# Optimization experiments

Hardware: AMD Instinct MI355X
Metric: run time of the kernel (lower is better)

Reference implementation:

```python
import jax, jax.numpy as jnp
import numpy as np

NUM_HEADS = 16
HEAD_SIZE = 64
CTXT_LEN = 2048
N_EMBED = 1024
BATCH = 2


def setup_inputs() -> dict:
    key = jax.random.key(0)
    ks = jax.random.split(key, 5)
    s = 0.02  # realistic init scale for weights
    return {
        "x": jax.random.normal(ks[0], (BATCH, CTXT_LEN, N_EMBED), dtype=jnp.float32),
        "Wk": jax.random.normal(ks[1], (N_EMBED, NUM_HEADS * HEAD_SIZE), dtype=jnp.float32) * s,
        "bk": jnp.zeros((NUM_HEADS * HEAD_SIZE,), dtype=jnp.float32),
        "Wq": jax.random.normal(ks[2], (N_EMBED, NUM_HEADS * HEAD_SIZE), dtype=jnp.float32) * s,
        "bq": jnp.zeros((NUM_HEADS * HEAD_SIZE,), dtype=jnp.float32),
        "Wv": jax.random.normal(ks[3], (N_EMBED, NUM_HEADS * HEAD_SIZE), dtype=jnp.float32) * s,
        "bv": jnp.zeros((NUM_HEADS * HEAD_SIZE,), dtype=jnp.float32),
        "Wo": jax.random.normal(ks[4], (NUM_HEADS * HEAD_SIZE, N_EMBED), dtype=jnp.float32) * s,
        "bo": jnp.zeros((N_EMBED,), dtype=jnp.float32),
    }


def reference(x, Wk, bk, Wq, bq, Wv, bv, Wo, bo):
    B, T, E = x.shape
    H, D = NUM_HEADS, HEAD_SIZE
    # QKV projections -> [B, T, H, D]
    k = (x @ Wk + bk).reshape(B, T, H, D)
    q = (x @ Wq + bq).reshape(B, T, H, D)
    v = (x @ Wv + bv).reshape(B, T, H, D)
    # NOTE: source scales by 1/sqrt(n_embed), not 1/sqrt(head_size)
    scale = 1.0 / (E ** 0.5)
    wei = jnp.einsum('bthd,bshd->bhts', q, k) * scale  # [B, H, T, T]
    causal = jnp.tril(jnp.ones((T, T), dtype=bool))
    wei = jnp.where(causal, wei, -jnp.inf)
    wei = jax.nn.softmax(wei, axis=-1)
    # dropout p=0.0 -> identity
    out = jnp.einsum('bhts,bshd->bthd', wei, v).reshape(B, T, H * D)
    return out @ Wo + bo
```

## Files before the change

### kernel.cpp

```cpp
#include <hip/hip_runtime.h>

#define NH 16
#define HS 64
#define T_CTX 2048
#define NE 1024
#define NB 2
#define BT (NB*T_CTX)
#define HD (NH*HS)

typedef unsigned short u16;
typedef __bf16 bf16_t;
typedef bf16_t bf16x8 __attribute__((ext_vector_type(8)));
typedef float f32x4 __attribute__((ext_vector_type(4)));
typedef u16 u16x8 __attribute__((ext_vector_type(8)));
typedef u16 u16x4 __attribute__((ext_vector_type(4)));

#define GLDS(gp, lp) __builtin_amdgcn_global_load_lds( \
    (const __attribute__((address_space(1))) void*)(gp), \
    (__attribute__((address_space(3))) void*)(lp), 16, 0, 0)

__device__ __forceinline__ u16 f2bf(float f) {
  union { float f; unsigned u; } x; x.f = f;
  return (u16)((x.u + 0x7fffu + ((x.u >> 16) & 1u)) >> 16);
}
__device__ __forceinline__ float bf2f(u16 u) {
  union { unsigned u; float f; } x; x.u = ((unsigned)u) << 16;
  return x.f;
}
__device__ __forceinline__ unsigned pack_bf2(float hi, float lo) {
  union { float f; unsigned u; } H, L; H.f = hi; L.f = lo;
  return __builtin_amdgcn_perm(H.u + 0x8000u, L.u + 0x8000u, 0x07060302);
}

__global__ __launch_bounds__(256) void k_prep_x(const float* __restrict__ x,
                                                u16* __restrict__ xb) {
  int i = blockIdx.x * blockDim.x + threadIdx.x;
  float4 v = ((const float4*)x)[i];
  ushort4 o;
  o.x = f2bf(v.x); o.y = f2bf(v.y); o.z = f2bf(v.z); o.w = f2bf(v.w);
  ((ushort4*)xb)[i] = o;
}

__global__ __launch_bounds__(256) void k_prep_w(
    const float* __restrict__ W0, const float* __restrict__ W1,
    const float* __restrict__ W2, const float* __restrict__ W3,
    u16* __restrict__ T0, u16* __restrict__ T1,
    u16* __restrict__ T2, u16* __restrict__ T3) {
  const float* W; u16* T;
  switch (blockIdx.z) {
    case 0: W = W0; T = T0; break;
    case 1: W = W1; T = T1; break;
    case 2: W = W2; T = T2; break;
    default: W = W3; T = T3; break;
  }
  __shared__ u16 tile[64 * 72];
  int k0 = blockIdx.x * 64, n0 = blockIdx.y * 64;
  int tid = threadIdx.x;
#pragma unroll
  for (int it = 0; it < 4; ++it) {
    int ci = tid + it * 256;
    int k = ci >> 4, c = ci & 15;
    float4 v = *(const float4*)&W[(size_t)(k0 + k) * NE + n0 + c * 4];
    int n = c * 4;
    tile[(n + 0) * 72 + k] = f2bf(v.x);
    tile[(n + 1) * 72 + k] = f2bf(v.y);
    tile[(n + 2) * 72 + k] = f2bf(v.z);
    tile[(n + 3) * 72 + k] = f2bf(v.w);
  }
  __syncthreads();
#pragma unroll
  for (int it = 0; it < 2; ++it) {
    int co = tid + it * 256;
    int n = co >> 3, c = co & 7;
    u16x8 v = *(const u16x8*)&tile[n * 72 + c * 8];
    *(u16x8*)&T[(size_t)(n0 + n) * NE + k0 + c * 8] = v;
  }
}

__device__ __forceinline__ void gemm_core(
    const u16* __restrict__ A, const u16* __restrict__ Bt,
    int m0, int n0, u16* As, u16* Bs, f32x4 (&acc)[4][4]) {
  const int tid = threadIdx.x, lane = tid & 63, w = tid >> 6;
  const int wm = (w >> 1) * 64, wn = (w & 1) * 64;
  const int q = lane >> 4, l16 = lane & 15;
#pragma unroll
  for (int i = 0; i < 4; ++i)
#pragma unroll
    for (int j = 0; j < 4; ++j)
#pragma unroll
      for (int r = 0; r < 4; ++r) acc[i][j][r] = 0.f;

  for (int k0 = 0; k0 < NE; k0 += 32) {
#pragma unroll
    for (int s2 = 0; s2 < 2; ++s2) {
      int ci = w * 64 + lane + s2 * 256;
      int row = ci >> 2, cc = ci & 3;
      GLDS(A  + (size_t)(m0 + row) * NE + k0 + cc * 8, As + (size_t)(w * 64 + s2 * 256) * 8);
      GLDS(Bt + (size_t)(n0 + row) * NE + k0 + cc * 8, Bs + (size_t)(w * 64 + s2 * 256) * 8);
    }
    __syncthreads();
    bf16x8 av[4], bv4[4];
#pragma unroll
    for (int i = 0; i < 4; ++i) av[i]  = *(const bf16x8*)&As[(wm + i * 16 + l16) * 32 + q * 8];
#pragma unroll
    for (int j = 0; j < 4; ++j) bv4[j] = *(const bf16x8*)&Bs[(wn + j * 16 + l16) * 32 + q * 8];
#pragma unroll
    for (int i = 0; i < 4; ++i)
#pragma unroll
      for (int j = 0; j < 4; ++j)
        acc[i][j] = __builtin_amdgcn_mfma_f32_16x16x32_bf16(av[i], bv4[j], acc[i][j], 0, 0, 0);
    __syncthreads();
  }
}

__global__ __launch_bounds__(256) void k_gemm_qkv(
    const u16* __restrict__ xb, const u16* __restrict__ Wt,
    const float* __restrict__ bq, const float* __restrict__ bk,
    const float* __restrict__ bv, u16* __restrict__ Qw,
    u16* __restrict__ Kw, u16* __restrict__ Vtw) {
  __shared__ u16 As[128 * 32], Bs[128 * 32];
  __shared__ u16 Es[128 * 132];
  const int z = blockIdx.z;
  const u16* W = Wt + (size_t)z * NE * HD;
  const float* bias = (z == 0) ? bq : (z == 1 ? bk : bv);
  const float scale = (z == 0) ? 0.03125f * 1.4426950408889634f : 1.0f;
  const int m0 = blockIdx.y * 128, n0 = blockIdx.x * 128;
  f32x4 acc[4][4];
  gemm_core(xb, W, m0, n0, As, Bs, acc);
  const int tid = threadIdx.x;
  const int lane = tid & 63, w = tid >> 6;
  const int wm = (w >> 1) * 64, wn = (w & 1) * 64, q = lane >> 4, l16 = lane & 15;
  const int bb = m0 >> 11;
  if (z == 2) {
#pragma unroll
    for (int j = 0; j < 4; ++j) {
      int n = wn + j * 16 + l16;
      float bn = bias[n0 + n];
#pragma unroll
      for (int i = 0; i < 4; ++i) {
        int m = wm + i * 16 + q * 4;
        u16x4 pk;
#pragma unroll
        for (int r = 0; r < 4; ++r) pk[r] = f2bf(acc[i][j][r] + bn);
        *(u16x4*)&Es[n * 132 + m] = pk;
      }
    }
    __syncthreads();
#pragma unroll
    for (int it = 0; it < 8; ++it) {
      int idx = it * 256 + tid;
      int dl = idx >> 4, c = idx & 15;
      u16x8 v = *(const u16x8*)&Es[dl * 132 + c * 8];
      int ng = n0 + dl, h = ng >> 6, d = ng & 63;
      int tt = (m0 & (T_CTX - 1)) + c * 8;
      *(u16x8*)&Vtw[((size_t)((bb * NH + h) * HS + d)) * T_CTX + tt] = v;
    }
  } else {
    u16* dst = (z == 0) ? Qw : Kw;
#pragma unroll
    for (int j = 0; j < 4; ++j) {
      int n = wn + j * 16 + l16;
      float bn = bias[n0 + n];
#pragma unroll
      for (int i = 0; i < 4; ++i)
#pragma unroll
        for (int r = 0; r < 4; ++r) {
          int m = wm + i * 16 + q * 4 + r;
          Es[m * 132 + n] = f2bf((acc[i][j][r] + bn) * scale);
        }
    }
    __syncthreads();
#pragma unroll
    for (int it = 0; it < 8; ++it) {
      int idx = it * 256 + tid;
      int tl = idx >> 4, c = idx & 15;
      u16x8 v = *(const u16x8*)&Es[tl * 132 + c * 8];
      int ng = n0 + c * 8, h = ng >> 6, d = ng & 63;
      int tt = (m0 & (T_CTX - 1)) + tl;
      *(u16x8*)&dst[(((size_t)(bb * NH + h)) * T_CTX + tt) * HS + d] = v;
    }
  }
}

__device__ __forceinline__ void stage_kv(const u16* __restrict__ Kp,
                                         const u16* __restrict__ Vp,
                                         int k0, u16* KsB, u16* VsB, int tid) {
#pragma unroll
  for (int it = 0; it < 2; ++it) {
    int ci = tid + it * 256;
    int row = ci >> 3, cc = ci & 7;
    int prow = (row & 32) | ((row & 12) << 1) | ((row & 16) >> 2) | (row & 3);
    int sw = (cc ^ (row & 7)) * 8;
    GLDS(Kp + (size_t)(k0 + prow) * HS + sw, KsB + ci * 8);
    GLDS(Vp + (size_t)row * T_CTX + k0 + sw, VsB + ci * 8);
  }
}

__global__ __launch_bounds__(256) void k_attn(
    const u16* __restrict__ Qw, const u16* __restrict__ Kw,
    const u16* __restrict__ Vtw, u16* __restrict__ op0,
    u16* __restrict__ op1, u16* __restrict__ op2,
    float* __restrict__ lsum) {
  __shared__ u16 Ks[3 * 64 * 64];
  __shared__ u16 Vs[3 * 64 * 64];

  const int bh = blockIdx.y;
  const int x = blockIdx.x;
  const int qt = 15 - x / 3;
  const int part = x - (15 - qt) * 3;
  const int ntiles = 2 * (qt + 1);
  const int npt = (ntiles + 2) / 3;
  const int klo = part * npt;
  const int khi = min(klo + npt, ntiles);
  const int qbase = qt * 128;

  const u16* Qp = Qw + (size_t)bh * T_CTX * HS;
  const u16* Kp = Kw + (size_t)bh * T_CTX * HS;
  const u16* Vp = Vtw + (size_t)bh * HS * T_CTX;

  const int tid = threadIdx.x, lane = tid & 63, w = tid >> 6;
  const int q = lane >> 4, c = lane & 15;
  const int rbase = w * 32;

  bf16x8 aq[2][2];
#pragma unroll
  for (int i = 0; i < 2; ++i)
#pragma unroll
    for (int s = 0; s < 2; ++s)
      aq[i][s] = *(const bf16x8*)&Qp[(size_t)(qbase + rbase + i * 16 + c) * HS + s * 32 + q * 8];

  f32x4 o[2][4];
  float lrow[2] = {0.f, 0.f};
#pragma unroll
  for (int i = 0; i < 2; ++i)
#pragma unroll
    for (int j = 0; j < 4; ++j)
#pragma unroll
      for (int r = 0; r < 4; ++r) o[i][j][r] = 0.f;

  if (klo < khi)     stage_kv(Kp, Vp, klo * 64,       Ks,        Vs,        tid);
  if (klo + 1 < khi) stage_kv(Kp, Vp, (klo + 1) * 64, Ks + 4096, Vs + 4096, tid);

  for (int kt = klo; kt < khi; ++kt) {
    const int k0 = kt * 64;
    const int idx = kt - klo;
    u16* KsB = Ks + (idx % 3) * 4096;
    u16* VsB = Vs + (idx % 3) * 4096;
    if (kt + 1 < khi) {
      asm volatile("s_waitcnt vmcnt(4)\n\ts_barrier" ::: "memory");
    } else {
      asm volatile("s_waitcnt vmcnt(0)\n\ts_barrier" ::: "memory");
    }
    if (kt + 2 < khi)
      stage_kv(Kp, Vp, (kt + 2) * 64,
               Ks + ((idx + 2) % 3) * 4096, Vs + ((idx + 2) % 3) * 4096, tid);

    f32x4 s[4][2];
#pragma unroll
    for (int i2 = 0; i2 < 4; ++i2) {
      int krow = i2 * 16 + c;
      bf16x8 kf0 = *(const bf16x8*)&KsB[krow * 64 + ((0 + q) ^ (krow & 7)) * 8];
      bf16x8 kf1 = *(const bf16x8*)&KsB[krow * 64 + ((4 + q) ^ (krow & 7)) * 8];
#pragma unroll
      for (int j2 = 0; j2 < 2; ++j2) {
        f32x4 z4 = {0.f, 0.f, 0.f, 0.f};
        z4 = __builtin_amdgcn_mfma_f32_16x16x32_bf16(kf0, aq[j2][0], z4, 0, 0, 0);
        s[i2][j2] = __builtin_amdgcn_mfma_f32_16x16x32_bf16(kf1, aq[j2][1], z4, 0, 0, 0);
      }
    }

    if (k0 + 63 > qbase + rbase) {
#pragma unroll
      for (int i2 = 0; i2 < 4; ++i2)
#pragma unroll
        for (int j2 = 0; j2 < 2; ++j2)
#pragma unroll
          for (int r = 0; r < 4; ++r) {
            int key = k0 + ((i2 >> 1) << 5) + (q << 3) + ((i2 & 1) << 2) + r;
            int qrow = qbase + rbase + j2 * 16 + c;
            if (key > qrow) s[i2][j2][r] = -1e30f;
          }
    }

#pragma unroll
    for (int i2 = 0; i2 < 4; ++i2)
#pragma unroll
      for (int j2 = 0; j2 < 2; ++j2)
#pragma unroll
        for (int r = 0; r < 4; ++r) {
          float p = __builtin_amdgcn_exp2f(s[i2][j2][r]);
          s[i2][j2][r] = p;
          lrow[j2] += p;
        }

#pragma unroll
    for (int ks = 0; ks < 2; ++ks) {
      bf16x8 bv4[4];
#pragma unroll
      for (int j = 0; j < 4; ++j) {
        int d = j * 16 + c;
        bv4[j] = *(const bf16x8*)&VsB[d * 64 + ((ks * 4 + q) ^ (d & 7)) * 8];
      }
#pragma unroll
      for (int i = 0; i < 2; ++i) {
        union { uint4 u; bf16x8 b; } af;
        af.u.x = pack_bf2(s[2 * ks][i][1],     s[2 * ks][i][0]);
        af.u.y = pack_bf2(s[2 * ks][i][3],     s[2 * ks][i][2]);
        af.u.z = pack_bf2(s[2 * ks + 1][i][1], s[2 * ks + 1][i][0]);
        af.u.w = pack_bf2(s[2 * ks + 1][i][3], s[2 * ks + 1][i][2]);
#pragma unroll
        for (int j = 0; j < 4; ++j)
          o[i][j] = __builtin_amdgcn_mfma_f32_16x16x32_bf16(af.b, bv4[j], o[i][j], 0, 0, 0);
      }
    }
  }

  u16* op = (part == 0) ? op0 : (part == 1 ? op1 : op2);
  const size_t row0 = (size_t)bh * T_CTX + qbase;
#pragma unroll
  for (int i = 0; i < 2; ++i) {
    lrow[i] += __shfl_xor(lrow[i], 16, 64);
    lrow[i] += __shfl_xor(lrow[i], 32, 64);
  }
  if (q == 0) {
#pragma unroll
    for (int i = 0; i < 2; ++i)
      lsum[(size_t)part * 65536 + row0 + rbase + i * 16 + c] = lrow[i];
  }
#pragma unroll
  for (int i = 0; i < 2; ++i)
#pragma unroll
    for (int r = 0; r < 4; ++r) {
      size_t t = row0 + rbase + i * 16 + q * 4 + r;
#pragma unroll
      for (int j = 0; j < 4; ++j)
        op[t * 64 + j * 16 + c] = f2bf(o[i][j][r]);
    }
}

__global__ __launch_bounds__(256) void k_combine(
    const u16* __restrict__ op0, const u16* __restrict__ op1,
    const u16* __restrict__ op2, const float* __restrict__ lsum,
    u16* __restrict__ att) {
  int idx = blockIdx.x * 256 + threadIdx.x;
  int row = idx >> 3, oct = idx & 7;
  float l0 = lsum[row], l1 = lsum[65536 + row], l2 = lsum[131072 + row];
  float inv = 1.f / (l0 + l1 + l2);
  u16x8 a = *(const u16x8*)&op0[(size_t)row * 64 + oct * 8];
  u16x8 b = *(const u16x8*)&op1[(size_t)row * 64 + oct * 8];
  u16x8 d = *(const u16x8*)&op2[(size_t)row * 64 + oct * 8];
  u16x8 ov;
#pragma unroll
  for (int e = 0; e < 8; ++e)
    ov[e] = f2bf((bf2f(a[e]) + bf2f(b[e]) + bf2f(d[e])) * inv);
  int bh = row >> 11, t = row & 2047, bb = bh >> 4, h = bh & 15;
  *(u16x8*)&att[((size_t)(bb * T_CTX + t)) * HD + h * 64 + oct * 8] = ov;
}

__global__ __launch_bounds__(256) void k_gemm_out(
    const u16* __restrict__ attb, const u16* __restrict__ Wot,
    const float* __restrict__ bo, float* __restrict__ out) {
  __shared__ u16 As[64 * 32], Bs[128 * 32];
  const int m0 = blockIdx.y * 64, n0 = blockIdx.x * 128;
  const int tid = threadIdx.x, lane = tid & 63, w = tid >> 6;
  const int wm = (w & 1) * 32, wn = (w >> 1) * 64;
  const int q = lane >> 4, l16 = lane & 15;
  f32x4 acc[2][4];
#pragma unroll
  for (int i = 0; i < 2; ++i)
#pragma unroll
    for (int j = 0; j < 4; ++j)
#pragma unroll
      for (int r = 0; r < 4; ++r) acc[i][j][r] = 0.f;

  for (int k0 = 0; k0 < NE; k0 += 32) {
    {
      int row = tid >> 2, cc = tid & 3;
      GLDS(attb + (size_t)(m0 + row) * NE + k0 + cc * 8, As + (size_t)tid * 8);
    }
#pragma unroll
    for (int s2 = 0; s2 < 2; ++s2) {
      int ci = tid + s2 * 256;
      int row = ci >> 2, cc = ci & 3;
      GLDS(Wot + (size_t)(n0 + row) * NE + k0 + cc * 8, Bs + (size_t)ci * 8);
    }
    __syncthreads();
    bf16x8 av[2], bv4[4];
#pragma unroll
    for (int i = 0; i < 2; ++i) av[i]  = *(const bf16x8*)&As[(wm + i * 16 + l16) * 32 + q * 8];
#pragma unroll
    for (int j = 0; j < 4; ++j) bv4[j] = *(const bf16x8*)&Bs[(wn + j * 16 + l16) * 32 + q * 8];
#pragma unroll
    for (int i = 0; i < 2; ++i)
#pragma unroll
      for (int j = 0; j < 4; ++j)
        acc[i][j] = __builtin_amdgcn_mfma_f32_16x16x32_bf16(av[i], bv4[j], acc[i][j], 0, 0, 0);
    __syncthreads();
  }
#pragma unroll
  for (int j = 0; j < 4; ++j) {
    int n = n0 + wn + j * 16 + l16;
    float bn = bo[n];
#pragma unroll
    for (int i = 0; i < 2; ++i)
#pragma unroll
      for (int r = 0; r < 4; ++r) {
        int m = m0 + wm + i * 16 + q * 4 + r;
        out[(size_t)m * NE + n] = acc[i][j][r] + bn;
      }
  }
}

extern "C" void kernel_launch(void* const* d_in, const int* in_sizes, int n_in,
                              void* d_out, int out_size, void* d_ws, size_t ws_size,
                              hipStream_t stream) {
  (void)in_sizes; (void)n_in; (void)out_size; (void)ws_size;
  const float* x  = (const float*)d_in[0];
  const float* Wk = (const float*)d_in[1];
  const float* bk = (const float*)d_in[2];
  const float* Wq = (const float*)d_in[3];
  const float* bq = (const float*)d_in[4];
  const float* Wv = (const float*)d_in[5];
  const float* bv = (const float*)d_in[6];
  const float* Wo = (const float*)d_in[7];
  const float* bo = (const float*)d_in[8];
  float* out = (float*)d_out;

  u16* base = (u16*)d_ws;
  const size_t M = 1024 * 1024;
  u16* xb   = base;
  u16* Wt   = base + 4 * M;
  u16* Wot  = base + 7 * M;
  u16* Qw   = base + 8 * M;
  u16* Kw   = base + 12 * M;
  u16* Vtw  = base + 16 * M;
  u16* op0  = base + 20 * M;
  u16* op1  = base + 24 * M;
  u16* op2  = base;
  float* lsum = (float*)(base + 4 * M);
  u16* attw = base + 12 * M;

  k_prep_x<<<dim3(BT * NE / 4 / 256), 256, 0, stream>>>(x, xb);
  k_prep_w<<<dim3(16, 16, 4), 256, 0, stream>>>(
      Wq, Wk, Wv, Wo, Wt, Wt + (size_t)NE * HD, Wt + (size_t)2 * NE * HD, Wot);
  k_gemm_qkv<<<dim3(8, 32, 3), 256, 0, stream>>>(xb, Wt, bq, bk, bv, Qw, Kw, Vtw);
  k_attn<<<dim3(48, 32), 256, 0, stream>>>(Qw, Kw, Vtw, op0, op1, op2, lsum);
  k_combine<<<dim3(2048), 256, 0, stream>>>(op0, op1, op2, lsum, attw);
  k_gemm_out<<<dim3(8, 64), 256, 0, stream>>>(attw, Wot, bo, out);
}
```

Before: 212.3 us.

## Triple-buffer LDS loads in QKV and output GEMMs with async prefetch

Replaces the single-buffered load/sync/compute loop in the QKV projection and output projection GEMMs with a three-stage LDS ring. Tiles are prefetched two k-steps ahead via global_load_lds, and each step waits with a partial vmcnt and one barrier instead of two __syncthreads. The goal is to overlap global memory latency with MFMA work. It uses more shared memory, which may lower occupancy, and relies on hand-counted vmcnt values staying correct.

```diff
diff --git a/kernel.cpp b/kernel.cpp
--- a/kernel.cpp
+++ b/kernel.cpp
@@ -77,59 +77,65 @@
   }
 }
 
-__device__ __forceinline__ void gemm_core(
-    const u16* __restrict__ A, const u16* __restrict__ Bt,
-    int m0, int n0, u16* As, u16* Bs, f32x4 (&acc)[4][4]) {
-  const int tid = threadIdx.x, lane = tid & 63, w = tid >> 6;
-  const int wm = (w >> 1) * 64, wn = (w & 1) * 64;
-  const int q = lane >> 4, l16 = lane & 15;
-#pragma unroll
-  for (int i = 0; i < 4; ++i)
-#pragma unroll
-    for (int j = 0; j < 4; ++j)
-#pragma unroll
-      for (int r = 0; r < 4; ++r) acc[i][j][r] = 0.f;
-
-  for (int k0 = 0; k0 < NE; k0 += 32) {
-#pragma unroll
-    for (int s2 = 0; s2 < 2; ++s2) {
-      int ci = w * 64 + lane + s2 * 256;
-      int row = ci >> 2, cc = ci & 3;
-      GLDS(A  + (size_t)(m0 + row) * NE + k0 + cc * 8, As + (size_t)(w * 64 + s2 * 256) * 8);
-      GLDS(Bt + (size_t)(n0 + row) * NE + k0 + cc * 8, Bs + (size_t)(w * 64 + s2 * 256) * 8);
-    }
-    __syncthreads();
-    bf16x8 av[4], bv4[4];
-#pragma unroll
-    for (int i = 0; i < 4; ++i) av[i]  = *(const bf16x8*)&As[(wm + i * 16 + l16) * 32 + q * 8];
-#pragma unroll
-    for (int j = 0; j < 4; ++j) bv4[j] = *(const bf16x8*)&Bs[(wn + j * 16 + l16) * 32 + q * 8];
-#pragma unroll
-    for (int i = 0; i < 4; ++i)
-#pragma unroll
-      for (int j = 0; j < 4; ++j)
-        acc[i][j] = __builtin_amdgcn_mfma_f32_16x16x32_bf16(av[i], bv4[j], acc[i][j], 0, 0, 0);
-    __syncthreads();
-  }
-}
-
 __global__ __launch_bounds__(256) void k_gemm_qkv(
     const u16* __restrict__ xb, const u16* __restrict__ Wt,
     const float* __restrict__ bq, const float* __restrict__ bk,
     const float* __restrict__ bv, u16* __restrict__ Qw,
     u16* __restrict__ Kw, u16* __restrict__ Vtw) {
-  __shared__ u16 As[128 * 32], Bs[128 * 32];
-  __shared__ u16 Es[128 * 132];
+  __shared__ u16 sh[3 * 8192];
   const int z = blockIdx.z;
   const u16* W = Wt + (size_t)z * NE * HD;
   const float* bias = (z == 0) ? bq : (z == 1 ? bk : bv);
   const float scale = (z == 0) ? 0.03125f * 1.4426950408889634f : 1.0f;
   const int m0 = blockIdx.y * 128, n0 = blockIdx.x * 128;
-  f32x4 acc[4][4];
-  gemm_core(xb, W, m0, n0, As, Bs, acc);
   const int tid = threadIdx.x;
   const int lane = tid & 63, w = tid >> 6;
   const int wm = (w >> 1) * 64, wn = (w & 1) * 64, q = lane >> 4, l16 = lane & 15;
+
+  auto stage = [&](int k0, int b) {
+    u16* As = sh + b * 8192;
+    u16* Bs = As + 4096;
+#pragma unroll
+    for (int s2 = 0; s2 < 2; ++s2) {
+      int ci = w * 64 + lane + s2 * 256;
+      int row = ci >> 2, cc = ci & 3;
+      GLDS(xb + (size_t)(m0 + row) * NE + k0 + cc * 8, As + (size_t)(w * 64 + s2 * 256) * 8);
+      GLDS(W  + (size_t)(n0 + row) * NE + k0 + cc * 8, Bs + (size_t)(w * 64 + s2 * 256) * 8);
+    }
+  };
+
+  f32x4 acc[4][4];
+#pragma unroll
+  for (int i = 0; i < 4; ++i)
+#pragma unroll
+    for (int j = 0; j < 4; ++j)
+#pragma unroll
+      for (int r = 0; r < 4; ++r) acc[i][j][r] = 0.f;
+
+  stage(0, 0);
+  stage(32, 1);
+  for (int kt = 0; kt < 32; ++kt) {
+    u16* As = sh + (kt % 3) * 8192;
+    u16* Bs = As + 4096;
+    if (kt + 1 < 32)
+      asm volatile("s_waitcnt vmcnt(4)\n\ts_barrier" ::: "memory");
+    else
+      asm volatile("s_waitcnt vmcnt(0)\n\ts_barrier" ::: "memory");
+    if (kt + 2 < 32) stage((kt + 2) * 32, (kt + 2) % 3);
+    bf16x8 av[4], bv4[4];
+#pragma unroll
+    for (int i = 0; i < 4; ++i) av[i]  = *(const bf16x8*)&As[(wm + i * 16 + l16) * 32 + q * 8];
+#pragma unroll
+    for (int j = 0; j < 4; ++j) bv4[j] = *(const bf16x8*)&Bs[(wn + j * 16 + l16) * 32 + q * 8];
+#pragma unroll
+    for (int i = 0; i < 4; ++i)
+#pragma unroll
+      for (int j = 0; j < 4; ++j)
+        acc[i][j] = __builtin_amdgcn_mfma_f32_16x16x32_bf16(av[i], bv4[j], acc[i][j], 0, 0, 0);
+  }
+  __syncthreads();
+  u16* Es = sh;
+
   const int bb = m0 >> 11;
   if (z == 2) {
 #pragma unroll
@@ -360,20 +366,15 @@
 __global__ __launch_bounds__(256) void k_gemm_out(
     const u16* __restrict__ attb, const u16* __restrict__ Wot,
     const float* __restrict__ bo, float* __restrict__ out) {
-  __shared__ u16 As[64 * 32], Bs[128 * 32];
+  __shared__ u16 sh[3 * 6144];
   const int m0 = blockIdx.y * 64, n0 = blockIdx.x * 128;
   const int tid = threadIdx.x, lane = tid & 63, w = tid >> 6;
   const int wm = (w & 1) * 32, wn = (w >> 1) * 64;
   const int q = lane >> 4, l16 = lane & 15;
-  f32x4 acc[2][4];
-#pragma unroll
-  for (int i = 0; i < 2; ++i)
-#pragma unroll
-    for (int j = 0; j < 4; ++j)
-#pragma unroll
-      for (int r = 0; r < 4; ++r) acc[i][j][r] = 0.f;
-
-  for (int k0 = 0; k0 < NE; k0 += 32) {
+
+  auto stage = [&](int k0, int b) {
+    u16* As = sh + b * 6144;
+    u16* Bs = As + 2048;
     {
       int row = tid >> 2, cc = tid & 3;
       GLDS(attb + (size_t)(m0 + row) * NE + k0 + cc * 8, As + (size_t)tid * 8);
@@ -384,7 +385,26 @@
       int row = ci >> 2, cc = ci & 3;
       GLDS(Wot + (size_t)(n0 + row) * NE + k0 + cc * 8, Bs + (size_t)ci * 8);
     }
-    __syncthreads();
+  };
+
+  f32x4 acc[2][4];
+#pragma unroll
+  for (int i = 0; i < 2; ++i)
+#pragma unroll
+    for (int j = 0; j < 4; ++j)
+#pragma unroll
+      for (int r = 0; r < 4; ++r) acc[i][j][r] = 0.f;
+
+  stage(0, 0);
+  stage(32, 1);
+  for (int kt = 0; kt < 32; ++kt) {
+    u16* As = sh + (kt % 3) * 6144;
+    u16* Bs = As + 2048;
+    if (kt + 1 < 32)
+      asm volatile("s_waitcnt vmcnt(3)\n\ts_barrier" ::: "memory");
+    else
+      asm volatile("s_waitcnt vmcnt(0)\n\ts_barrier" ::: "memory");
+    if (kt + 2 < 32) stage((kt + 2) * 32, (kt + 2) % 3);
     bf16x8 av[2], bv4[4];
 #pragma unroll
     for (int i = 0; i < 2; ++i) av[i]  = *(const bf16x8*)&As[(wm + i * 16 + l16) * 32 + q * 8];
@@ -395,7 +415,6 @@
 #pragma unroll
       for (int j = 0; j < 4; ++j)
         acc[i][j] = __builtin_amdgcn_mfma_f32_16x16x32_bf16(av[i], bv4[j], acc[i][j], 0, 0, 0);
-    __syncthreads();
   }
 #pragma unroll
   for (int j = 0; j < 4; ++j) {
```

Result: faster. 201.8 us (-4.9%).
